# Optimization experiments

Measured on AMD Instinct MI355X. Metric: run time of the kernel, lower is better.

## Reference

```python
import jax, jax.numpy as jnp
import numpy as np

N_HEADS = 16
N_UNITS = 1024
B, S = 4, 1024


def setup_inputs() -> dict:
    key = jax.random.key(0)
    ks = jax.random.split(key, 12)
    std = 0.02
    query = jax.random.normal(ks[0], (B, S, N_UNITS), dtype=jnp.float32)
    key_t = jax.random.normal(ks[1], (B, S, N_UNITS), dtype=jnp.float32)
    value = jax.random.normal(ks[2], (B, S, N_UNITS), dtype=jnp.float32)
    # causal mask [B, S, S]; forward does mask.unsqueeze(1) -> broadcast over heads
    mask = jnp.broadcast_to(jnp.tril(jnp.ones((S, S), dtype=jnp.int32)), (B, S, S))
    Wq = jax.random.normal(ks[3], (N_UNITS, N_UNITS), dtype=jnp.float32) * std
    bq = jnp.zeros((N_UNITS,), dtype=jnp.float32)
    Wk = jax.random.normal(ks[4], (N_UNITS, N_UNITS), dtype=jnp.float32) * std
    bk = jnp.zeros((N_UNITS,), dtype=jnp.float32)
    Wv = jax.random.normal(ks[5], (N_UNITS, N_UNITS), dtype=jnp.float32) * std
    bv = jnp.zeros((N_UNITS,), dtype=jnp.float32)
    Wo = jax.random.normal(ks[6], (N_UNITS, N_UNITS), dtype=jnp.float32) * std
    bo = jnp.zeros((N_UNITS,), dtype=jnp.float32)
    return {"query": query, "key": key_t, "value": value, "mask": mask,
            "Wq": Wq, "bq": bq, "Wk": Wk, "bk": bk, "Wv": Wv, "bv": bv,
            "Wo": Wo, "bo": bo}


def reference(query, key, value, mask, Wq, bq, Wk, bk, Wv, bv, Wo, bo):
    b, s, u = query.shape
    h = N_HEADS
    dk = u // h
    # projections (torch Linear: x @ W.T + b), split into heads -> [b, h, s, dk]
    q = (query @ Wq.T + bq).reshape(b, s, h, dk).transpose(0, 2, 1, 3)
    k = (key @ Wk.T + bk).reshape(b, s, h, dk).transpose(0, 2, 1, 3)
    v = (value @ Wv.T + bv).reshape(b, s, h, dk).transpose(0, 2, 1, 3)
    # NOTE: original divides by sqrt(d_k) twice -> net scale 1/d_k (faithful)
    scores = jnp.einsum('bhqd,bhkd->bhqk', q, k) / jnp.float32(dk)
    scores = jnp.where(mask[:, None, :, :] == 0, jnp.float32(-1e9), scores)
    attn = jax.nn.softmax(scores, axis=-1)  # dropout = identity (eval mode)
    out = jnp.einsum('bhqk,bhkd->bhqd', attn, v)
    out = out.transpose(0, 2, 1, 3).reshape(b, s, u)
    return out @ Wo.T + bo
```

## Files before the change

### kernel.cpp

```cpp
#include <hip/hip_runtime.h>
#include <stdint.h>

#define NH 16
#define DK 64
#define NB 4
#define SS 1024
#define UU 1024

typedef __attribute__((ext_vector_type(8))) __bf16 bf16x8;
typedef __attribute__((ext_vector_type(4))) float f32x4;

__device__ inline short f2bf(float f) {
  union { float f; uint32_t u; } c; c.f = f;
  uint32_t u = c.u;
  uint32_t r = (u + 0x7fffu + ((u >> 16) & 1u)) >> 16;
  return (short)(uint16_t)r;
}

__global__ void cvt_multi(const float* __restrict__ s0, const float* __restrict__ s1,
                          const float* __restrict__ s2, const float* __restrict__ s3,
                          short* __restrict__ dst, int n4each) {
  const int z = blockIdx.z;
  const float* s = (z == 0) ? s0 : (z == 1) ? s1 : (z == 2) ? s2 : s3;
  int i = blockIdx.x * blockDim.x + threadIdx.x;
  if (i >= n4each) return;
  const float4 v = reinterpret_cast<const float4*>(s)[i];
  short4 o;
  o.x = f2bf(v.x); o.y = f2bf(v.y); o.z = f2bf(v.z); o.w = f2bf(v.w);
  reinterpret_cast<short4*>(dst + (size_t)z * n4each * 4)[i] = o;
}

template <int ROWS>
__device__ inline void stage_rows(short* lds, const short* gsrc, int ld) {
  const int t = threadIdx.x;
  const int w = t >> 6;
  constexpr int ROUNDS = ROWS / 64;
#pragma unroll
  for (int r = 0; r < ROUNDS; ++r) {
    int idx = r * 256 + t;
    const short* src = gsrc + (size_t)(idx >> 2) * ld + (idx & 3) * 8;
    __builtin_amdgcn_global_load_lds(
        (const __attribute__((address_space(1))) void*)src,
        (__attribute__((address_space(3))) void*)(lds + (size_t)(r * 256 + (w << 6)) * 8),
        16, 0, 0);
  }
}

#define BK 32
#define QSCALE 0.015625f


#define STAGEQ(BI)                                                            \
  {                                                                           \
    stage_rows<128>(AsAll + ((BI) % 3) * (128 * BK), Abf + (size_t)m0 * UU + (BI) * BK, UU); \
    stage_rows<128>(BsAll + ((BI) % 3) * (128 * BK), Bt + (BI) * BK, UU);     \
  }

#define BODYQ(BI, VMC, ...)                                                   \
  {                                                                           \
    asm volatile("s_waitcnt vmcnt(" VMC ")" ::: "memory");                    \
    __builtin_amdgcn_sched_barrier(0);                                        \
    __builtin_amdgcn_s_barrier();                                             \
    __builtin_amdgcn_sched_barrier(0);                                        \
    __VA_ARGS__                                                               \
    __builtin_amdgcn_sched_barrier(0);                                        \
    {                                                                         \
      const short* AsC_ = AsAll + ((BI) % 3) * (128 * BK);                    \
      const short* BsC_ = BsAll + ((BI) % 3) * (128 * BK);                    \
      bf16x8 af[4], bfr[4];                                                   \
      _Pragma("unroll") for (int i = 0; i < 4; ++i)                           \
          af[i] = *(const bf16x8*)&AsC_[(wr * 64 + i * 16 + lr) * BK + lg * 8]; \
      _Pragma("unroll") for (int j = 0; j < 4; ++j)                           \
          bfr[j] = *(const bf16x8*)&BsC_[(wc * 64 + j * 16 + lr) * BK + lg * 8]; \
      _Pragma("unroll") for (int i = 0; i < 4; ++i)                           \
          _Pragma("unroll") for (int j = 0; j < 4; ++j)                       \
              acc[i][j] = __builtin_amdgcn_mfma_f32_16x16x32_bf16(af[i], bfr[j], acc[i][j], 0, 0, 0); \
    }                                                                         \
  }

__global__ void gemm_qkv(const short* __restrict__ xq, const short* __restrict__ xk,
                         const short* __restrict__ xv, const short* __restrict__ wq,
                         const short* __restrict__ wk, const short* __restrict__ wv,
                         const float* __restrict__ bq, const float* __restrict__ bk,
                         const float* __restrict__ bv, short* __restrict__ qb,
                         short* __restrict__ kb, short* __restrict__ vT) {
  __shared__ short AsAll[3 * 128 * BK];
  __shared__ short BsAll[3 * 128 * BK];
  const int bid = blockIdx.x;
  const int g = bid & 7, s2 = bid >> 3;
  const int P = g + (s2 >> 3) * 8;
  const int xt = s2 & 7;
  const int which = P >> 5;
  const int m0 = (P & 31) * 128;
  const int n0 = xt * 128;

  const short* Abf = (which == 0) ? xq : (which == 1) ? xk : xv;
  const short* Bt = ((which == 0) ? wq : (which == 1) ? wk : wv) + (size_t)n0 * UU;
  const float* bias = (which == 0) ? bq : (which == 1) ? bk : bv;

  const int t = threadIdx.x;
  const int w = t >> 6, l = t & 63, lg = l >> 4, lr = l & 15;
  const int wr = w >> 1, wc = w & 1;

  f32x4 acc[4][4];
#pragma unroll
  for (int i = 0; i < 4; ++i)
#pragma unroll
    for (int j = 0; j < 4; ++j) acc[i][j] = (f32x4){0.f, 0.f, 0.f, 0.f};

  STAGEQ(0);
  STAGEQ(1);
  for (int bi = 0; bi < 30; ++bi) {
    BODYQ(bi, "4", STAGEQ(bi + 2);)
  }
  BODYQ(30, "4", ;)
  BODYQ(31, "0", ;)

#pragma unroll
  for (int i = 0; i < 4; ++i) {
#pragma unroll
    for (int j = 0; j < 4; ++j) {
      const int col = n0 + wc * 64 + j * 16 + lr;
      const float bv2 = bias[col];
#pragma unroll
      for (int r = 0; r < 4; ++r) {
        const int row = m0 + wr * 64 + i * 16 + lg * 4 + r;
        float v = acc[i][j][r] + bv2;
        if (which == 0) v *= QSCALE;
        const int b = row >> 10, s = row & 1023;
        const int h = col >> 6, d = col & 63;
        if (which < 2) {
          short* outp = (which == 0) ? qb : kb;
          outp[((size_t)(b * NH + h) * SS + s) * DK + d] = f2bf(v);
        } else {
          vT[((size_t)(b * NH + h) * DK + d) * SS + s] = f2bf(v);
        }
      }
    }
  }
}

#define STAGEO(BI)                                                            \
  {                                                                           \
    stage_rows<128>(AsAll + ((BI) % 3) * (128 * BK), A + (size_t)m0 * K + (BI) * BK, K); \
    stage_rows<64>(BsAll3 + ((BI) % 3) * (64 * BK), Bt + (size_t)n0 * K + (BI) * BK, K); \
  }

#define BODYO(BI, VMC, ...)                                                   \
  {                                                                           \
    asm volatile("s_waitcnt vmcnt(" VMC ")" ::: "memory");                    \
    __builtin_amdgcn_sched_barrier(0);                                        \
    __builtin_amdgcn_s_barrier();                                             \
    __builtin_amdgcn_sched_barrier(0);                                        \
    __VA_ARGS__                                                               \
    __builtin_amdgcn_sched_barrier(0);                                        \
    {                                                                         \
      const short* AsC_ = AsAll + ((BI) % 3) * (128 * BK);                    \
      const short* BsC_ = BsAll3 + ((BI) % 3) * (64 * BK);                    \
      bf16x8 af[4], bfr[2];                                                   \
      _Pragma("unroll") for (int i = 0; i < 4; ++i)                           \
          af[i] = *(const bf16x8*)&AsC_[(wr * 64 + i * 16 + lr) * BK + lg * 8]; \
      _Pragma("unroll") for (int j = 0; j < 2; ++j)                           \
          bfr[j] = *(const bf16x8*)&BsC_[(wc * 32 + j * 16 + lr) * BK + lg * 8]; \
      _Pragma("unroll") for (int i = 0; i < 4; ++i)                           \
          _Pragma("unroll") for (int j = 0; j < 2; ++j)                       \
              acc[i][j] = __builtin_amdgcn_mfma_f32_16x16x32_bf16(af[i], bfr[j], acc[i][j], 0, 0, 0); \
    }                                                                         \
  }

__global__ void gemm_out(const short* __restrict__ A, const short* __restrict__ Bt,
                         const float* __restrict__ bias, float* __restrict__ out,
                         int M, int N, int K) {
  __shared__ short AsAll[3 * 128 * BK];
  __shared__ short BsAll3[3 * 64 * BK];
  const int bid = blockIdx.x;
  const int g = bid & 7, s2 = bid >> 3;
  const int y = g + (s2 >> 4) * 8;
  const int xt = s2 & 15;
  const int m0 = y * 128, n0 = xt * 64;

  const int t = threadIdx.x;
  const int w = t >> 6, l = t & 63, lg = l >> 4, lr = l & 15;
  const int wr = w >> 1, wc = w & 1;

  f32x4 acc[4][2];
#pragma unroll
  for (int i = 0; i < 4; ++i)
#pragma unroll
    for (int j = 0; j < 2; ++j) acc[i][j] = (f32x4){0.f, 0.f, 0.f, 0.f};

  STAGEO(0);
  STAGEO(1);
  for (int bi = 0; bi < 30; ++bi) {
    BODYO(bi, "3", STAGEO(bi + 2);)
  }
  BODYO(30, "3", ;)
  BODYO(31, "0", ;)

#pragma unroll
  for (int i = 0; i < 4; ++i) {
#pragma unroll
    for (int j = 0; j < 2; ++j) {
      const int col = n0 + wc * 32 + j * 16 + lr;
      const float bv = bias[col];
#pragma unroll
      for (int r = 0; r < 4; ++r) {
        const int row = m0 + wr * 64 + i * 16 + lg * 4 + r;
        out[(size_t)row * N + col] = acc[i][j][r] + bv;
      }
    }
  }
}

__global__ void attn_fused(const short* __restrict__ Qh, const short* __restrict__ Kh,
                           const short* __restrict__ VT, short* __restrict__ Ctx) {
  __shared__ short Ks[2][4096];
  __shared__ short Vs[2][4096];
  __shared__ short Pl[4][1024];

  const int bid = blockIdx.x;
  const int g = bid & 7, s2 = bid >> 3;
  const int bh = g + (s2 >> 3) * 8;
  const int xp = s2 & 7;

  const int t = threadIdx.x;
  const int w = t >> 6, l = t & 63, lg = l >> 4, lr = l & 15;
  const short* Qp = Qh + (size_t)bh * SS * DK;
  const short* Kp = Kh + (size_t)bh * SS * DK;
  const short* Vp = VT + (size_t)bh * DK * SS;
  short* Pw = Pl[w];
  const int b = bh >> 4, h = bh & 15;
  const int rowloc = w * 16 + lg * 4;

  int lofs[2], gofK[2], gofV[2];
#pragma unroll
  for (int r = 0; r < 2; ++r) {
    const int idx = r * 256 + t;
    const int L = idx << 4;
    const int Lp = L ^ (((L >> 7) & 7) << 4);
    lofs[r] = (r * 256 + (w << 6)) * 8;
    gofK[r] = (Lp >> 7) * DK + ((Lp & 127) >> 1);
    gofV[r] = (Lp >> 7) * SS + ((Lp & 127) >> 1);
  }

  for (int half = 0; half < 2; ++half) {
    const int qt = half ? (15 - xp) : xp;
    const int q0 = qt * 64 + w * 16;
    const int nt = qt + 1;

    bf16x8 qf[2];
#pragma unroll
    for (int c = 0; c < 2; ++c)
      qf[c] = *(const bf16x8*)&Qp[(q0 + lr) * DK + c * 32 + lg * 8];

    f32x4 o[4];
    float lsum[4];
#pragma unroll
    for (int i = 0; i < 4; ++i) { o[i] = (f32x4){0.f, 0.f, 0.f, 0.f}; lsum[i] = 0.f; }

#pragma unroll
    for (int r = 0; r < 2; ++r)
      __builtin_amdgcn_global_load_lds(
          (const __attribute__((address_space(1))) void*)(Kp + gofK[r]),
          (__attribute__((address_space(3))) void*)(Ks[0] + lofs[r]), 16, 0, 0);
#pragma unroll
    for (int r = 0; r < 2; ++r)
      __builtin_amdgcn_global_load_lds(
          (const __attribute__((address_space(1))) void*)(Vp + gofV[r]),
          (__attribute__((address_space(3))) void*)(Vs[0] + lofs[r]), 16, 0, 0);

    for (int tt = 0; tt < nt; ++tt) {
      const int cb = tt & 1, nb = cb ^ 1;
      if (tt + 1 < nt) {
        const size_t koff = (size_t)(tt + 1) * 64;
#pragma unroll
        for (int r = 0; r < 2; ++r)
          __builtin_amdgcn_global_load_lds(
              (const __attribute__((address_space(1))) void*)(Kp + koff * DK + gofK[r]),
              (__attribute__((address_space(3))) void*)(Ks[nb] + lofs[r]), 16, 0, 0);
#pragma unroll
        for (int r = 0; r < 2; ++r)
          __builtin_amdgcn_global_load_lds(
              (const __attribute__((address_space(1))) void*)(Vp + koff + gofV[r]),
              (__attribute__((address_space(3))) void*)(Vs[nb] + lofs[r]), 16, 0, 0);
        asm volatile("s_waitcnt vmcnt(4)" ::: "memory");
      } else {
        asm volatile("s_waitcnt vmcnt(0)" ::: "memory");
      }
      __builtin_amdgcn_sched_barrier(0);
      __builtin_amdgcn_s_barrier();
      __builtin_amdgcn_sched_barrier(0);

      const short* Kt = Ks[cb];
      const short* Vt = Vs[cb];

      f32x4 sacc[4];
#pragma unroll
      for (int nf = 0; nf < 4; ++nf) sacc[nf] = (f32x4){0.f, 0.f, 0.f, 0.f};
#pragma unroll
      for (int nf = 0; nf < 4; ++nf)
#pragma unroll
        for (int c = 0; c < 2; ++c) {
          const int row = nf * 16 + lr;
          const int Lb = (row << 7) + c * 64 + lg * 16;
          bf16x8 kf = *(const bf16x8*)((const char*)Kt + (Lb ^ ((row & 7) << 4)));
          sacc[nf] = __builtin_amdgcn_mfma_f32_16x16x32_bf16(qf[c], kf, sacc[nf], 0, 0, 0);
        }

      const bool diag = (tt == qt);
#pragma unroll
      for (int nf = 0; nf < 4; ++nf) {
        const int colloc = nf * 16 + lr;
#pragma unroll
        for (int r = 0; r < 4; ++r) {
          float s = sacc[nf][r];
          if (diag && colloc > (rowloc + r)) s = -1.0e9f;
          float p = __expf(s);
          lsum[r] += p;
          const int prow = lg * 4 + r;
          const int boff = (prow * 128 + colloc * 2) ^ ((prow & 7) << 4);
          Pw[boff >> 1] = f2bf(p);
        }
      }

      asm volatile("s_waitcnt lgkmcnt(0)" ::: "memory");
      __builtin_amdgcn_sched_barrier(0);

      bf16x8 pf[2];
#pragma unroll
      for (int c2 = 0; c2 < 2; ++c2) {
        const int boff = (lr * 128 + (c2 * 32 + lg * 8) * 2) ^ ((lr & 7) << 4);
        pf[c2] = *(const bf16x8*)((const char*)Pw + boff);
      }
#pragma unroll
      for (int df = 0; df < 4; ++df)
#pragma unroll
        for (int c2 = 0; c2 < 2; ++c2) {
          const int row = df * 16 + lr;
          const int Lb = (row << 7) + c2 * 64 + lg * 16;
          bf16x8 vf = *(const bf16x8*)((const char*)Vt + (Lb ^ ((row & 7) << 4)));
          o[df] = __builtin_amdgcn_mfma_f32_16x16x32_bf16(pf[c2], vf, o[df], 0, 0, 0);
        }
      __builtin_amdgcn_sched_barrier(0);
      __builtin_amdgcn_s_barrier();
    }

#pragma unroll
    for (int r = 0; r < 4; ++r) {
#pragma unroll
      for (int d = 1; d < 16; d <<= 1)
        lsum[r] += __shfl_xor(lsum[r], d, 64);
    }
    float inv[4];
#pragma unroll
    for (int r = 0; r < 4; ++r) inv[r] = 1.0f / lsum[r];
#pragma unroll
    for (int df = 0; df < 4; ++df)
#pragma unroll
      for (int r = 0; r < 4; ++r) {
        const int qg = q0 + lg * 4 + r;
        Ctx[((size_t)(b * SS + qg)) * UU + h * DK + df * 16 + lr] = f2bf(o[df][r] * inv[r]);
      }
  }
}

extern "C" void kernel_launch(void* const* d_in, const int* in_sizes, int n_in,
                              void* d_out, int out_size, void* d_ws, size_t ws_size,
                              hipStream_t stream) {
  const float* query = (const float*)d_in[0];
  const float* key   = (const float*)d_in[1];
  const float* value = (const float*)d_in[2];
  const float* Wq = (const float*)d_in[4];
  const float* bq = (const float*)d_in[5];
  const float* Wk = (const float*)d_in[6];
  const float* bk = (const float*)d_in[7];
  const float* Wv = (const float*)d_in[8];
  const float* bv = (const float*)d_in[9];
  const float* Wo = (const float*)d_in[10];
  const float* bo = (const float*)d_in[11];
  float* out = (float*)d_out;

  char* ws = (char*)d_ws;
  const size_t MT = (size_t)NB * SS;
  short* qb  = (short*)ws;
  short* kb  = qb + MT * UU;
  short* vT  = kb + MT * UU;
  short* ctx = vT + MT * UU;
  short* xq  = ctx + MT * UU;
  short* xk  = xq + MT * UU;
  short* xv  = xk + MT * UU;
  short* wq  = xv + MT * UU;
  short* wk  = wq + (size_t)UU * UU;
  short* wv  = wk + (size_t)UU * UU;
  short* wo  = wv + (size_t)UU * UU;

  const int TPB = 256;
  {
    int n4 = (int)(MT * UU / 4);
    hipLaunchKernelGGL(cvt_multi, dim3(n4 / TPB, 1, 3), dim3(TPB), 0, stream,
                       query, key, value, query, xq, n4);
  }
  {
    int n4 = (int)((size_t)UU * UU / 4);
    hipLaunchKernelGGL(cvt_multi, dim3(n4 / TPB, 1, 4), dim3(TPB), 0, stream,
                       Wq, Wk, Wv, Wo, wq, n4);
  }

  hipLaunchKernelGGL(gemm_qkv, dim3(768), dim3(TPB), 0, stream,
                     xq, xk, xv, wq, wk, wv, bq, bk, bv, qb, kb, vT);

  hipLaunchKernelGGL(attn_fused, dim3(512), dim3(TPB), 0, stream, qb, kb, vT, ctx);

  hipLaunchKernelGGL(gemm_out, dim3(512), dim3(TPB), 0, stream,
                     ctx, wo, bo, out, (int)MT, UU, UU);
}
```

Baseline: 214.8 us.

## Double attention query tile per block and merge conversion kernels into one launch

The attention kernel now gives each wave 32 query rows (two MFMA fragments), so a block covers 128 queries and reuses each staged K/V tile twice as much. The grid halves to 256 blocks, and the causal mask uses global column and row indices per fragment. s_setprio is raised around the MFMA sections. The two fp32-to-bf16 conversion launches are merged into one kernel over the contiguous workspace. The trade-offs are fewer resident blocks and waves, higher register and LDS use, and extra fully-masked work on the last key tiles.

```diff
diff --git a/kernel.cpp b/kernel.cpp
--- a/kernel.cpp
+++ b/kernel.cpp
@@ -17,17 +17,27 @@
   return (short)(uint16_t)r;
 }
 
-__global__ void cvt_multi(const float* __restrict__ s0, const float* __restrict__ s1,
-                          const float* __restrict__ s2, const float* __restrict__ s3,
-                          short* __restrict__ dst, int n4each) {
-  const int z = blockIdx.z;
-  const float* s = (z == 0) ? s0 : (z == 1) ? s1 : (z == 2) ? s2 : s3;
-  int i = blockIdx.x * blockDim.x + threadIdx.x;
-  if (i >= n4each) return;
-  const float4 v = reinterpret_cast<const float4*>(s)[i];
+__global__ void cvt_all(const float* __restrict__ q, const float* __restrict__ k,
+                        const float* __restrict__ v, const float* __restrict__ wq,
+                        const float* __restrict__ wk, const float* __restrict__ wv,
+                        const float* __restrict__ wo, short* __restrict__ dst) {
+  const int i = blockIdx.x * blockDim.x + threadIdx.x;
+  const float* s;
+  int local;
+  if (i < 3 * 1048576) {
+    const int z = i >> 20;
+    local = i & 1048575;
+    s = (z == 0) ? q : (z == 1) ? k : v;
+  } else {
+    const int j = i - 3 * 1048576;
+    const int z = j >> 18;
+    local = j & 262143;
+    s = (z == 0) ? wq : (z == 1) ? wk : (z == 2) ? wv : wo;
+  }
+  const float4 vv = reinterpret_cast<const float4*>(s)[local];
   short4 o;
-  o.x = f2bf(v.x); o.y = f2bf(v.y); o.z = f2bf(v.z); o.w = f2bf(v.w);
-  reinterpret_cast<short4*>(dst + (size_t)z * n4each * 4)[i] = o;
+  o.x = f2bf(vv.x); o.y = f2bf(vv.y); o.z = f2bf(vv.z); o.w = f2bf(vv.w);
+  reinterpret_cast<short4*>(dst)[i] = o;
 }
 
 template <int ROWS>
@@ -48,7 +58,6 @@
 
 #define BK 32
 #define QSCALE 0.015625f
-
 
 #define STAGEQ(BI)                                                            \
   {                                                                           \
@@ -216,12 +225,12 @@
                            const short* __restrict__ VT, short* __restrict__ Ctx) {
   __shared__ short Ks[2][4096];
   __shared__ short Vs[2][4096];
-  __shared__ short Pl[4][1024];
+  __shared__ short Pl[4][2048];
 
   const int bid = blockIdx.x;
   const int g = bid & 7, s2 = bid >> 3;
-  const int bh = g + (s2 >> 3) * 8;
-  const int xp = s2 & 7;
+  const int bh = g + (s2 >> 2) * 8;
+  const int xp = s2 & 3;
 
   const int t = threadIdx.x;
   const int w = t >> 6, l = t & 63, lg = l >> 4, lr = l & 15;
@@ -230,7 +239,6 @@
   const short* Vp = VT + (size_t)bh * DK * SS;
   short* Pw = Pl[w];
   const int b = bh >> 4, h = bh & 15;
-  const int rowloc = w * 16 + lg * 4;
 
   int lofs[2], gofK[2], gofV[2];
 #pragma unroll
@@ -244,19 +252,23 @@
   }
 
   for (int half = 0; half < 2; ++half) {
-    const int qt = half ? (15 - xp) : xp;
-    const int q0 = qt * 64 + w * 16;
-    const int nt = qt + 1;
-
-    bf16x8 qf[2];
-#pragma unroll
-    for (int c = 0; c < 2; ++c)
-      qf[c] = *(const bf16x8*)&Qp[(q0 + lr) * DK + c * 32 + lg * 8];
-
-    f32x4 o[4];
-    float lsum[4];
-#pragma unroll
-    for (int i = 0; i < 4; ++i) { o[i] = (f32x4){0.f, 0.f, 0.f, 0.f}; lsum[i] = 0.f; }
+    const int qt = half ? (7 - xp) : xp;
+    const int q0 = qt * 128 + w * 32;
+    const int nt = 2 * qt + 2;
+
+    bf16x8 qf[2][2];
+#pragma unroll
+    for (int f = 0; f < 2; ++f)
+#pragma unroll
+      for (int c = 0; c < 2; ++c)
+        qf[f][c] = *(const bf16x8*)&Qp[(q0 + f * 16 + lr) * DK + c * 32 + lg * 8];
+
+    f32x4 o[2][4];
+    float lsum[2][4];
+#pragma unroll
+    for (int f = 0; f < 2; ++f)
+#pragma unroll
+      for (int i = 0; i < 4; ++i) { o[f][i] = (f32x4){0.f, 0.f, 0.f, 0.f}; lsum[f][i] = 0.f; }
 
 #pragma unroll
     for (int r = 0; r < 2; ++r)
@@ -270,6 +282,7 @@
           (__attribute__((address_space(3))) void*)(Vs[0] + lofs[r]), 16, 0, 0);
 
     for (int tt = 0; tt < nt; ++tt) {
+      const int kk0 = tt * 64;
       const int cb = tt & 1, nb = cb ^ 1;
       if (tt + 1 < nt) {
         const size_t koff = (size_t)(tt + 1) * 64;
@@ -294,9 +307,12 @@
       const short* Kt = Ks[cb];
       const short* Vt = Vs[cb];
 
-      f32x4 sacc[4];
-#pragma unroll
-      for (int nf = 0; nf < 4; ++nf) sacc[nf] = (f32x4){0.f, 0.f, 0.f, 0.f};
+      f32x4 sacc[2][4];
+#pragma unroll
+      for (int f = 0; f < 2; ++f)
+#pragma unroll
+        for (int nf = 0; nf < 4; ++nf) sacc[f][nf] = (f32x4){0.f, 0.f, 0.f, 0.f};
+      __builtin_amdgcn_s_setprio(1);
 #pragma unroll
       for (int nf = 0; nf < 4; ++nf)
 #pragma unroll
@@ -304,63 +320,79 @@
           const int row = nf * 16 + lr;
           const int Lb = (row << 7) + c * 64 + lg * 16;
           bf16x8 kf = *(const bf16x8*)((const char*)Kt + (Lb ^ ((row & 7) << 4)));
-          sacc[nf] = __builtin_amdgcn_mfma_f32_16x16x32_bf16(qf[c], kf, sacc[nf], 0, 0, 0);
+#pragma unroll
+          for (int f = 0; f < 2; ++f)
+            sacc[f][nf] = __builtin_amdgcn_mfma_f32_16x16x32_bf16(qf[f][c], kf, sacc[f][nf], 0, 0, 0);
         }
-
-      const bool diag = (tt == qt);
-#pragma unroll
-      for (int nf = 0; nf < 4; ++nf) {
-        const int colloc = nf * 16 + lr;
-#pragma unroll
-        for (int r = 0; r < 4; ++r) {
-          float s = sacc[nf][r];
-          if (diag && colloc > (rowloc + r)) s = -1.0e9f;
-          float p = __expf(s);
-          lsum[r] += p;
-          const int prow = lg * 4 + r;
-          const int boff = (prow * 128 + colloc * 2) ^ ((prow & 7) << 4);
-          Pw[boff >> 1] = f2bf(p);
+      __builtin_amdgcn_s_setprio(0);
+
+#pragma unroll
+      for (int f = 0; f < 2; ++f) {
+        const int frow = q0 + f * 16;
+        const bool diag = (kk0 + 63 > frow);
+#pragma unroll
+        for (int nf = 0; nf < 4; ++nf) {
+          const int colg = kk0 + nf * 16 + lr;
+#pragma unroll
+          for (int r = 0; r < 4; ++r) {
+            float s = sacc[f][nf][r];
+            if (diag && colg > (frow + lg * 4 + r)) s = -1.0e9f;
+            float p = __expf(s);
+            lsum[f][r] += p;
+            const int prow = f * 16 + lg * 4 + r;
+            const int boff = (prow * 128 + (nf * 16 + lr) * 2) ^ ((prow & 7) << 4);
+            Pw[boff >> 1] = f2bf(p);
+          }
         }
       }
 
       asm volatile("s_waitcnt lgkmcnt(0)" ::: "memory");
       __builtin_amdgcn_sched_barrier(0);
 
-      bf16x8 pf[2];
-#pragma unroll
-      for (int c2 = 0; c2 < 2; ++c2) {
-        const int boff = (lr * 128 + (c2 * 32 + lg * 8) * 2) ^ ((lr & 7) << 4);
-        pf[c2] = *(const bf16x8*)((const char*)Pw + boff);
-      }
-#pragma unroll
-      for (int df = 0; df < 4; ++df)
+      __builtin_amdgcn_s_setprio(1);
+#pragma unroll
+      for (int f = 0; f < 2; ++f) {
+        bf16x8 pf[2];
 #pragma unroll
         for (int c2 = 0; c2 < 2; ++c2) {
-          const int row = df * 16 + lr;
-          const int Lb = (row << 7) + c2 * 64 + lg * 16;
-          bf16x8 vf = *(const bf16x8*)((const char*)Vt + (Lb ^ ((row & 7) << 4)));
-          o[df] = __builtin_amdgcn_mfma_f32_16x16x32_bf16(pf[c2], vf, o[df], 0, 0, 0);
+          const int prow = f * 16 + lr;
+          const int boff = (prow * 128 + (c2 * 32 + lg * 8) * 2) ^ ((prow & 7) << 4);
+          pf[c2] = *(const bf16x8*)((const char*)Pw + boff);
         }
+#pragma unroll
+        for (int df = 0; df < 4; ++df)
+#pragma unroll
+          for (int c2 = 0; c2 < 2; ++c2) {
+            const int row = df * 16 + lr;
+            const int Lb = (row << 7) + c2 * 64 + lg * 16;
+            bf16x8 vf = *(const bf16x8*)((const char*)Vt + (Lb ^ ((row & 7) << 4)));
+            o[f][df] = __builtin_amdgcn_mfma_f32_16x16x32_bf16(pf[c2], vf, o[f][df], 0, 0, 0);
+          }
+      }
+      __builtin_amdgcn_s_setprio(0);
       __builtin_amdgcn_sched_barrier(0);
       __builtin_amdgcn_s_barrier();
     }
 
 #pragma unroll
-    for (int r = 0; r < 4; ++r) {
-#pragma unroll
-      for (int d = 1; d < 16; d <<= 1)
-        lsum[r] += __shfl_xor(lsum[r], d, 64);
+    for (int f = 0; f < 2; ++f) {
+#pragma unroll
+      for (int r = 0; r < 4; ++r) {
+#pragma unroll
+        for (int d = 1; d < 16; d <<= 1)
+          lsum[f][r] += __shfl_xor(lsum[f][r], d, 64);
+      }
+      float inv[4];
+#pragma unroll
+      for (int r = 0; r < 4; ++r) inv[r] = 1.0f / lsum[f][r];
+#pragma unroll
+      for (int df = 0; df < 4; ++df)
+#pragma unroll
+        for (int r = 0; r < 4; ++r) {
+          const int qg = q0 + f * 16 + lg * 4 + r;
+          Ctx[((size_t)(b * SS + qg)) * UU + h * DK + df * 16 + lr] = f2bf(o[f][df][r] * inv[r]);
+        }
     }
-    float inv[4];
-#pragma unroll
-    for (int r = 0; r < 4; ++r) inv[r] = 1.0f / lsum[r];
-#pragma unroll
-    for (int df = 0; df < 4; ++df)
-#pragma unroll
-      for (int r = 0; r < 4; ++r) {
-        const int qg = q0 + lg * 4 + r;
-        Ctx[((size_t)(b * SS + qg)) * UU + h * DK + df * 16 + lr] = f2bf(o[df][r] * inv[r]);
-      }
   }
 }
 
@@ -395,21 +427,13 @@
   short* wo  = wv + (size_t)UU * UU;
 
   const int TPB = 256;
-  {
-    int n4 = (int)(MT * UU / 4);
-    hipLaunchKernelGGL(cvt_multi, dim3(n4 / TPB, 1, 3), dim3(TPB), 0, stream,
-                       query, key, value, query, xq, n4);
-  }
-  {
-    int n4 = (int)((size_t)UU * UU / 4);
-    hipLaunchKernelGGL(cvt_multi, dim3(n4 / TPB, 1, 4), dim3(TPB), 0, stream,
-                       Wq, Wk, Wv, Wo, wq, n4);
-  }
+  hipLaunchKernelGGL(cvt_all, dim3(4194304 / TPB), dim3(TPB), 0, stream,
+                     query, key, value, Wq, Wk, Wv, Wo, xq);
 
   hipLaunchKernelGGL(gemm_qkv, dim3(768), dim3(TPB), 0, stream,
                      xq, xk, xv, wq, wk, wv, bq, bk, bv, qb, kb, vT);
 
-  hipLaunchKernelGGL(attn_fused, dim3(512), dim3(TPB), 0, stream, qb, kb, vT, ctx);
+  hipLaunchKernelGGL(attn_fused, dim3(256), dim3(TPB), 0, stream, qb, kb, vT, ctx);
 
   hipLaunchKernelGGL(gemm_out, dim3(512), dim3(TPB), 0, stream,
                      ctx, wo, bo, out, (int)MT, UU, UU);
```

Measured after the change: 257.3 us. 1.2x slower.
